# Kernel optimization log

Measured on AMD Instinct MI355X. Metric: run time of the kernel, lower is better.

Reference implementation:

```python
import jax, jax.numpy as jnp
import numpy as np

N, E = 20000, 320000
IN, OUT, H1, H2 = 256, 32, 8, 1
NEG_SLOPE = 0.2


def _gatv2(x, src, dst, Wsrc, bsrc, Wdst, bdst, attn, Wres, bres, heads, dout):
    n = x.shape[0]
    fs = (x @ Wsrc + bsrc).reshape(n, heads, dout)   # (N,H,D)
    fd = (x @ Wdst + bdst).reshape(n, heads, dout)   # (N,H,D)
    # GATv2: leaky_relu BEFORE the attention dot product
    e = jax.nn.leaky_relu(fs[src] + fd[dst], NEG_SLOPE)      # (E,H,D)
    logits = jnp.einsum('ehd,hd->eh', e, attn)               # (E,H)
    # edge softmax over destination-node segments
    m = jax.ops.segment_max(logits, dst, num_segments=n)     # (N,H)
    ex = jnp.exp(logits - m[dst])
    s = jax.ops.segment_sum(ex, dst, num_segments=n)         # (N,H)
    alpha = ex / s[dst]                                      # (E,H)
    msg = alpha[:, :, None] * fs[src]                        # (E,H,D)
    out = jax.ops.segment_sum(msg, dst, num_segments=n)      # (N,H,D)
    res = (x @ Wres + bres).reshape(n, heads, dout)          # residual (dims differ -> Linear)
    return out + res


def setup_inputs() -> dict:
    key = jax.random.key(0)
    ks = jax.random.split(key, 16)
    sc = lambda fin: 1.0 / np.sqrt(fin)
    d = {}
    d['x'] = jax.random.normal(ks[0], (N, IN), jnp.float32)
    d['src'] = jax.random.randint(ks[1], (E,), 0, N, jnp.int32)
    d['dst'] = jax.random.randint(ks[2], (E,), 0, N, jnp.int32)
    # layer 1: IN -> OUT*H1
    d['Wsrc1'] = jax.random.normal(ks[3], (IN, OUT * H1), jnp.float32) * sc(IN)
    d['bsrc1'] = jnp.zeros((OUT * H1,), jnp.float32)
    d['Wdst1'] = jax.random.normal(ks[4], (IN, OUT * H1), jnp.float32) * sc(IN)
    d['bdst1'] = jnp.zeros((OUT * H1,), jnp.float32)
    d['attn1'] = jax.random.normal(ks[5], (H1, OUT), jnp.float32) * sc(OUT)
    d['Wres1'] = jax.random.normal(ks[6], (IN, OUT * H1), jnp.float32) * sc(IN)
    d['bres1'] = jnp.zeros((OUT * H1,), jnp.float32)
    # layer 2: OUT*H1 -> OUT, 1 head
    D2 = OUT * H1
    d['Wsrc2'] = jax.random.normal(ks[7], (D2, OUT * H2), jnp.float32) * sc(D2)
    d['bsrc2'] = jnp.zeros((OUT * H2,), jnp.float32)
    d['Wdst2'] = jax.random.normal(ks[8], (D2, OUT * H2), jnp.float32) * sc(D2)
    d['bdst2'] = jnp.zeros((OUT * H2,), jnp.float32)
    d['attn2'] = jax.random.normal(ks[9], (H2, OUT), jnp.float32) * sc(OUT)
    d['Wres2'] = jax.random.normal(ks[10], (D2, OUT * H2), jnp.float32) * sc(D2)
    d['bres2'] = jnp.zeros((OUT * H2,), jnp.float32)
    return d


def reference(x, src, dst,
              Wsrc1, bsrc1, Wdst1, bdst1, attn1, Wres1, bres1,
              Wsrc2, bsrc2, Wdst2, bdst2, attn2, Wres2, bres2):
    y = _gatv2(x, src, dst, Wsrc1, bsrc1, Wdst1, bdst1, attn1, Wres1, bres1, H1, OUT)
    y = jax.nn.relu(y)                       # (N, 8, OUT)
    y = y.reshape(x.shape[0], -1)            # (N, 8*OUT)
    y = _gatv2(y, src, dst, Wsrc2, bsrc2, Wdst2, bdst2, attn2, Wres2, bres2, H2, OUT)
    return y                                  # (N, 1, OUT)
```

## Files before the change

kernel.cpp:

```cpp
#include <hip/hip_runtime.h>
#include <hip/hip_bf16.h>

#define N_NODES 20000
#define N_PAD   20096
#define N_EDGES 320000
#define D_IN    256
#define NEG     0.2f
#define MAXDEG  64
#define NSB     64
#define EPSB    5000
#define NBIN    313

typedef __attribute__((ext_vector_type(8))) short short8;
typedef __attribute__((ext_vector_type(4))) float f32x4;
typedef __attribute__((ext_vector_type(4))) unsigned short u16x4;

__device__ __forceinline__ unsigned short f2b(float f) {
    unsigned int u = __float_as_uint(f);
    unsigned int r = (u + 0x7FFFu + ((u >> 16) & 1u)) >> 16;
    return (unsigned short)r;
}
__device__ __forceinline__ float b2f(unsigned short u) {
    union { unsigned int i; float f; } v;
    v.i = ((unsigned int)u) << 16;
    return v.f;
}

__device__ __forceinline__ void gload16(const void* g, void* l) {
    __builtin_amdgcn_global_load_lds((const __attribute__((address_space(1))) void*)g,
                                     (__attribute__((address_space(3))) void*)l, 16, 0, 0);
}

#define PB1 2512
#define PB2 3280
#define PB3 3376
#define PB4 3440
#define PREP_BLOCKS 3488
__global__ __launch_bounds__(256) void k_prep(
    const float* __restrict__ x, unsigned short* __restrict__ xb,
    const float* __restrict__ Ws1, const float* __restrict__ Wd1, const float* __restrict__ Wr1,
    unsigned short* __restrict__ wt,
    const float* __restrict__ Ws2, const float* __restrict__ Wd2, const float* __restrict__ Wr2,
    unsigned short* __restrict__ wt2,
    const int* __restrict__ dst, int* __restrict__ blockhist,
    unsigned short* __restrict__ yb)
{
    int bid = blockIdx.x, tid = threadIdx.x;
    if (bid < PB1) {
        int i = bid * 256 + tid;
        int row = i >> 5, c8 = (i & 31) * 8;
        short8 v = {0, 0, 0, 0, 0, 0, 0, 0};
        if (row < N_NODES) {
            float4 a = *reinterpret_cast<const float4*>(x + (size_t)row * 256 + c8);
            float4 b = *reinterpret_cast<const float4*>(x + (size_t)row * 256 + c8 + 4);
            v[0] = (short)f2b(a.x); v[1] = (short)f2b(a.y); v[2] = (short)f2b(a.z); v[3] = (short)f2b(a.w);
            v[4] = (short)f2b(b.x); v[5] = (short)f2b(b.y); v[6] = (short)f2b(b.z); v[7] = (short)f2b(b.w);
        }
        *reinterpret_cast<short8*>(xb + (size_t)row * 256 + c8) = v;
    } else if (bid < PB2) {
        int n = bid - PB1, k = tid;
        const float* W = (n < 256) ? Ws1 : ((n < 512) ? Wd1 : Wr1);
        int c = n & 255;
        wt[(size_t)n * 256 + k] = f2b(W[(size_t)k * 256 + c]);
    } else if (bid < PB3) {
        int n = bid - PB2, k = tid;
        const float* W = (n < 32) ? Ws2 : ((n < 64) ? Wd2 : Wr2);
        int c = n & 31;
        wt2[(size_t)n * 256 + (k ^ ((n & 7) << 3))] = f2b(W[(size_t)k * 32 + c]);
    } else if (bid < PB4) {
        __shared__ int hist[NBIN];
        int blk = bid - PB3;
        for (int b = tid; b < NBIN; b += 256) hist[b] = 0;
        __syncthreads();
        for (int it = 0; it < 20; ++it) {
            int li = it * 256 + tid;
            if (li < EPSB) atomicAdd(&hist[dst[blk * EPSB + li] >> 6], 1);
        }
        __syncthreads();
        for (int b = tid; b < NBIN; b += 256) blockhist[blk * NBIN + b] = hist[b];
    } else {
        int j = (bid - PB4) * 256 + tid;
        ((unsigned int*)(yb + (size_t)N_NODES * 256))[j] = 0u;
    }
}

__global__ __launch_bounds__(320) void k_pass3(
    const int* __restrict__ src, const int* __restrict__ dst,
    const int* __restrict__ blockhist,
    unsigned long long* __restrict__ sorted,
    int* __restrict__ binbase_g, int* __restrict__ bintotal_g)
{
    __shared__ int tmp[320];
    __shared__ int binbase[NBIN];
    __shared__ int rank[NBIN];
    int blk = blockIdx.x, tid = threadIdx.x;
    int mystart = 0, total = 0;
    if (tid < NBIN) {
        for (int b = 0; b < NSB; ++b) {
            int v = blockhist[b * NBIN + tid];
            total += v;
            if (b < blk) mystart += v;
        }
    }
    tmp[tid] = (tid < NBIN) ? total : 0;
    __syncthreads();
    for (int off = 1; off < 320; off <<= 1) {
        int v = (tid >= off) ? tmp[tid - off] : 0;
        __syncthreads();
        tmp[tid] += v;
        __syncthreads();
    }
    if (tid < NBIN) {
        int excl = tmp[tid] - total;
        binbase[tid] = excl;
        rank[tid] = mystart;
        if (blk == 0) { binbase_g[tid] = excl; bintotal_g[tid] = total; }
    }
    __syncthreads();
    for (int it = 0; it < 16; ++it) {
        int li = it * 320 + tid;
        if (li < EPSB) {
            int e = blk * EPSB + li;
            int d = dst[e];
            int b = d >> 6;
            int r = atomicAdd(&rank[b], 1);
            sorted[binbase[b] + r] = ((unsigned long long)(unsigned)d << 32) | (unsigned)src[e];
        }
    }
}

#define GEMM1_BLOCKS 1884
#define PASS4_BLOCKS 313
__global__ __launch_bounds__(256) void k_gemm_l1_mfma(
    const unsigned short* __restrict__ xb,
    const unsigned short* __restrict__ wt,
    const float* __restrict__ bs, const float* __restrict__ bd, const float* __restrict__ br,
    unsigned short* __restrict__ fs, unsigned short* __restrict__ fd, unsigned short* __restrict__ res,
    const unsigned long long* __restrict__ sorted,
    const int* __restrict__ binbase_g, const int* __restrict__ bintotal_g,
    int* __restrict__ colp, int* __restrict__ cnt)
{
    __shared__ __align__(16) unsigned short SH[12288];
    int t = threadIdx.x;
    int bid = blockIdx.x;

    if (bid >= GEMM1_BLOCKS) {
        int* ch = (int*)SH;
        int nb2 = bid - GEMM1_BLOCKS;
        if (t < 64) ch[t] = 0;
        __syncthreads();
        int base = binbase_g[nb2], tot = bintotal_g[nb2];
        for (int i = t; i < tot; i += 256) {
            unsigned long long p = sorted[base + i];
            int d = (int)(p >> 32);
            int s = (int)(p & 0xffffffffULL);
            int r = atomicAdd(&ch[d & 63], 1);
            if (r < MAXDEG) colp[(size_t)d * MAXDEG + r] = s;
        }
        __syncthreads();
        int node = nb2 * 64 + t;
        if (t < 64 && node < N_NODES) cnt[node] = ch[t];
        return;
    }

    int lane = t & 63, w = t >> 6;
    const int q = 235, r = 4;
    int xcd = bid & 7, slot = bid >> 3;
    int wg = (xcd < r ? xcd * (q + 1) : r * (q + 1) + (xcd - r) * q) + slot;
    int mb = wg / 6, nb = wg % 6;
    int row0 = mb * 64;
    int which = nb >> 1;
    int col0 = (nb & 1) * 128;
    int ncol0 = nb * 128;
    unsigned short* out = (which == 0) ? fs : ((which == 1) ? fd : res);
    const float* bias   = (which == 0) ? bs : ((which == 1) ? bd : br);

    auto stage = [&](int buf, int k0) {
        char* base = (char*)SH + buf * 12288;
        {
            int c = t, row = c >> 2, kc = (c & 3) * 8;
            gload16(xb + (size_t)(row0 + row) * 256 + k0 + kc, base + c * 16);
        }
#pragma unroll
        for (int r2 = 0; r2 < 2; r2++) {
            int c = r2 * 256 + t, row = c >> 2, kc = (c & 3) * 8;
            gload16(wt + (size_t)(ncol0 + row) * 256 + k0 + kc, base + 4096 + c * 16);
        }
    };

    f32x4 acc[4][2] = {};

    stage(0, 0);
    __syncthreads();
    int cur = 0;
#pragma unroll
    for (int it = 0; it < 8; ++it) {
        if (it < 7) stage(cur ^ 1, (it + 1) * 32);
        const char* Ab = (const char*)SH + cur * 12288;
        const char* Bb = Ab + 4096;
        short8 a[4], b[2];
#pragma unroll
        for (int m = 0; m < 4; m++)
            a[m] = *reinterpret_cast<const short8*>(Ab + ((m * 16 + (lane & 15)) * 64 + (lane >> 4) * 16));
#pragma unroll
        for (int n = 0; n < 2; n++)
            b[n] = *reinterpret_cast<const short8*>(Bb + ((w * 32 + n * 16 + (lane & 15)) * 64 + (lane >> 4) * 16));
#pragma unroll
        for (int m = 0; m < 4; m++)
#pragma unroll
            for (int n = 0; n < 2; n++)
                acc[m][n] = __builtin_amdgcn_mfma_f32_16x16x32_bf16(a[m], b[n], acc[m][n], 0, 0, 0);
        __syncthreads();
        cur ^= 1;
    }

    int cgrp = lane >> 4, ccol = lane & 15;
    float bvals[2];
#pragma unroll
    for (int n = 0; n < 2; n++) bvals[n] = bias[col0 + w * 32 + n * 16 + ccol];

#pragma unroll
    for (int m = 0; m < 4; m++)
#pragma unroll
        for (int n = 0; n < 2; n++)
#pragma unroll
            for (int q2 = 0; q2 < 4; q2++) {
                int lr = m * 16 + cgrp * 4 + q2;
                int cb = (w * 32 + n * 16 + ccol) * 2;
                int addr = lr * 256 + (cb ^ (cgrp << 5));
                *(unsigned short*)((char*)SH + addr) = f2b(acc[m][n][q2] + bvals[n]);
            }
    __syncthreads();
#pragma unroll
    for (int it = 0; it < 4; it++) {
        int lr = it * 16 + (t >> 4);
        int cb = (t & 15) * 16;
        short8 v = *(const short8*)((const char*)SH + (lr * 256 + (cb ^ (((lr >> 2) & 3) << 5))));
        int gr = row0 + lr;
        if (gr < N_NODES)
            *reinterpret_cast<short8*>(out + (size_t)gr * 256 + col0 + (t & 15) * 8) = v;
    }
}

__global__ __launch_bounds__(64) void k_gather_l1(
    const int* __restrict__ cnt, const int* __restrict__ colp,
    const unsigned short* __restrict__ fs1, const unsigned short* __restrict__ fd1,
    const unsigned short* __restrict__ res1, const float* __restrict__ attn1,
    unsigned short* __restrict__ y)
{
    int n = blockIdx.x;
    int l = threadIdx.x;
    u16x4 fdv4 = *reinterpret_cast<const u16x4*>(fd1 + (size_t)n * 256 + l * 4);
    float fdv[4] = {b2f(fdv4[0]), b2f(fdv4[1]), b2f(fdv4[2]), b2f(fdv4[3])};
    float4 attv = *reinterpret_cast<const float4*>(attn1 + l * 4);
    float att[4] = {attv.x, attv.y, attv.z, attv.w};

    const int* colrow = colp + (size_t)n * MAXDEG;
    int deg = cnt[n];
    if (deg > MAXDEG) deg = MAXDEG;

    float mA = -1e30f, sA = 0.f, aA[4] = {0.f, 0.f, 0.f, 0.f};
    float mB = -1e30f, sB = 0.f, aB[4] = {0.f, 0.f, 0.f, 0.f};

    int cA0 = (0 < deg) ? colrow[0] : 0;
    int cB0 = (1 < deg) ? colrow[1] : 0;
    int cA1 = (2 < deg) ? colrow[2] : 0;
    int cB1 = (3 < deg) ? colrow[3] : 0;
    u16x4 fA  = *reinterpret_cast<const u16x4*>(fs1 + (size_t)cA0 * 256 + l * 4);
    u16x4 fB  = *reinterpret_cast<const u16x4*>(fs1 + (size_t)cB0 * 256 + l * 4);
    u16x4 fA2 = *reinterpret_cast<const u16x4*>(fs1 + (size_t)cA1 * 256 + l * 4);
    u16x4 fB2 = *reinterpret_cast<const u16x4*>(fs1 + (size_t)cB1 * 256 + l * 4);

    int idx = 0;
    for (; idx + 1 < deg; idx += 2) {
        u16x4 vA = fA, vB = fB;
        fA = fA2; fB = fB2;
        int nA = (idx + 4 < deg) ? colrow[idx + 4] : 0;
        int nB = (idx + 5 < deg) ? colrow[idx + 5] : 0;
        fA2 = *reinterpret_cast<const u16x4*>(fs1 + (size_t)nA * 256 + l * 4);
        fB2 = *reinterpret_cast<const u16x4*>(fs1 + (size_t)nB * 256 + l * 4);

        float xa0 = b2f(vA[0]), xa1 = b2f(vA[1]), xa2 = b2f(vA[2]), xa3 = b2f(vA[3]);
        float ta0 = xa0 + fdv[0]; ta0 = ta0 > 0.f ? ta0 : NEG * ta0;
        float ta1 = xa1 + fdv[1]; ta1 = ta1 > 0.f ? ta1 : NEG * ta1;
        float ta2 = xa2 + fdv[2]; ta2 = ta2 > 0.f ? ta2 : NEG * ta2;
        float ta3 = xa3 + fdv[3]; ta3 = ta3 > 0.f ? ta3 : NEG * ta3;
        float pA = ta0 * att[0] + ta1 * att[1] + ta2 * att[2] + ta3 * att[3];
        float xb0 = b2f(vB[0]), xb1 = b2f(vB[1]), xb2 = b2f(vB[2]), xb3 = b2f(vB[3]);
        float tb0 = xb0 + fdv[0]; tb0 = tb0 > 0.f ? tb0 : NEG * tb0;
        float tb1 = xb1 + fdv[1]; tb1 = tb1 > 0.f ? tb1 : NEG * tb1;
        float tb2 = xb2 + fdv[2]; tb2 = tb2 > 0.f ? tb2 : NEG * tb2;
        float tb3 = xb3 + fdv[3]; tb3 = tb3 > 0.f ? tb3 : NEG * tb3;
        float pB = tb0 * att[0] + tb1 * att[1] + tb2 * att[2] + tb3 * att[3];

        pA += __shfl_xor(pA, 1); pB += __shfl_xor(pB, 1);
        pA += __shfl_xor(pA, 2); pB += __shfl_xor(pB, 2);
        pA += __shfl_xor(pA, 4); pB += __shfl_xor(pB, 4);

        float mnA = fmaxf(mA, pA);
        float eA  = __expf(pA - mnA);
        float scA = __expf(mA - mnA);
        sA = sA * scA + eA;
        aA[0] = aA[0] * scA + eA * xa0;
        aA[1] = aA[1] * scA + eA * xa1;
        aA[2] = aA[2] * scA + eA * xa2;
        aA[3] = aA[3] * scA + eA * xa3;
        mA = mnA;

        float mnB = fmaxf(mB, pB);
        float eB  = __expf(pB - mnB);
        float scB = __expf(mB - mnB);
        sB = sB * scB + eB;
        aB[0] = aB[0] * scB + eB * xb0;
        aB[1] = aB[1] * scB + eB * xb1;
        aB[2] = aB[2] * scB + eB * xb2;
        aB[3] = aB[3] * scB + eB * xb3;
        mB = mnB;
    }
    if (idx < deg) {
        float xa0 = b2f(fA[0]), xa1 = b2f(fA[1]), xa2 = b2f(fA[2]), xa3 = b2f(fA[3]);
        float ta0 = xa0 + fdv[0]; ta0 = ta0 > 0.f ? ta0 : NEG * ta0;
        float ta1 = xa1 + fdv[1]; ta1 = ta1 > 0.f ? ta1 : NEG * ta1;
        float ta2 = xa2 + fdv[2]; ta2 = ta2 > 0.f ? ta2 : NEG * ta2;
        float ta3 = xa3 + fdv[3]; ta3 = ta3 > 0.f ? ta3 : NEG * ta3;
        float pA = ta0 * att[0] + ta1 * att[1] + ta2 * att[2] + ta3 * att[3];
        pA += __shfl_xor(pA, 1);
        pA += __shfl_xor(pA, 2);
        pA += __shfl_xor(pA, 4);
        float mnA = fmaxf(mA, pA);
        float eA  = __expf(pA - mnA);
        float scA = __expf(mA - mnA);
        sA = sA * scA + eA;
        aA[0] = aA[0] * scA + eA * xa0;
        aA[1] = aA[1] * scA + eA * xa1;
        aA[2] = aA[2] * scA + eA * xa2;
        aA[3] = aA[3] * scA + eA * xa3;
        mA = mnA;
    }
    float mn = fmaxf(mA, mB);
    float scA = __expf(mA - mn), scB = __expf(mB - mn);
    float s = sA * scA + sB * scB;
    float a0 = aA[0] * scA + aB[0] * scB;
    float a1 = aA[1] * scA + aB[1] * scB;
    float a2 = aA[2] * scA + aB[2] * scB;
    float a3 = aA[3] * scA + aB[3] * scB;

    u16x4 rv4 = *reinterpret_cast<const u16x4*>(res1 + (size_t)n * 256 + l * 4);
    float inv = (s > 0.f) ? 1.f / s : 0.f;
    u16x4 o;
    o[0] = f2b(fmaxf(a0 * inv + b2f(rv4[0]), 0.f));
    o[1] = f2b(fmaxf(a1 * inv + b2f(rv4[1]), 0.f));
    o[2] = f2b(fmaxf(a2 * inv + b2f(rv4[2]), 0.f));
    o[3] = f2b(fmaxf(a3 * inv + b2f(rv4[3]), 0.f));
    *reinterpret_cast<u16x4*>(y + (size_t)n * 256 + l * 4) = o;
}

__global__ __launch_bounds__(256) void k_gemm_l2_mfma(
    const unsigned short* __restrict__ yb,
    const unsigned short* __restrict__ wt2,
    const float* __restrict__ bs, const float* __restrict__ bd, const float* __restrict__ br,
    unsigned short* __restrict__ fs2, unsigned short* __restrict__ fd2, unsigned short* __restrict__ res2)
{
    __shared__ __align__(16) unsigned short Bs[96 * 256];
    __shared__ __align__(16) unsigned short As[2][64 * 32];
    int t = threadIdx.x;
    int lane = t & 63, w = t >> 6;
    int row0 = blockIdx.x * 64;

    auto stage_a = [&](int buf, int k0) {
        int c = t;
        int row = c >> 2, kc = (c & 3) * 8;
        gload16(yb + (size_t)(row0 + row) * 256 + k0 + kc, (char*)As[buf] + c * 16);
    };

#pragma unroll
    for (int i = 0; i < 12; i++) {
        int c = i * 256 + t;
        gload16(wt2 + (size_t)c * 8, (char*)Bs + (size_t)c * 16);
    }
    stage_a(0, 0);
    __syncthreads();

    f32x4 acc[6] = {};
    int arow0 = w * 16;
    int cur = 0;

#pragma unroll
    for (int it = 0; it < 8; ++it) {
        if (it < 7) stage_a(cur ^ 1, (it + 1) * 32);
        short8 a = *reinterpret_cast<const short8*>((const char*)As[cur] + ((arow0 + (lane & 15)) * 64 + (lane >> 4) * 16));
        short8 b[6];
#pragma unroll
        for (int n = 0; n < 6; n++) {
            int brow = n * 16 + (lane & 15);
            int kbyte = (it * 32 + (lane >> 4) * 8) * 2;
            b[n] = *reinterpret_cast<const short8*>((const char*)Bs + (brow * 512 + (kbyte ^ ((brow & 7) << 4))));
        }
#pragma unroll
        for (int n = 0; n < 6; n++)
            acc[n] = __builtin_amdgcn_mfma_f32_16x16x32_bf16(a, b[n], acc[n], 0, 0, 0);
        __syncthreads();
        cur ^= 1;
    }

    int cgrp = lane >> 4, ccol = lane & 15;
#pragma unroll
    for (int n = 0; n < 6; n++) {
        int which = n >> 1;
        int cc = (n & 1) * 16 + ccol;
        unsigned short* out = (which == 0) ? fs2 : ((which == 1) ? fd2 : res2);
        const float* bias   = (which == 0) ? bs  : ((which == 1) ? bd  : br);
        float bv = bias[cc];
        int rbase = row0 + arow0 + cgrp * 4;
#pragma unroll
        for (int q2 = 0; q2 < 4; q2++) {
            int rr = rbase + q2;
            if (rr < N_NODES) out[(size_t)rr * 32 + cc] = f2b(acc[n][q2] + bv);
        }
    }
}

__global__ __launch_bounds__(64) void k_gather_l2(
    const int* __restrict__ cnt, const int* __restrict__ colp,
    const unsigned short* __restrict__ fs2, const unsigned short* __restrict__ fd2,
    const unsigned short* __restrict__ res2, const float* __restrict__ attn2,
    float* __restrict__ out)
{
    int n = blockIdx.x;
    int l = threadIdx.x;
    int d = l & 31, h = l >> 5;
    float fdv = b2f(fd2[(size_t)n * 32 + d]);
    float att = attn2[d];
    const int* colrow = colp + (size_t)n * MAXDEG;
    int deg = cnt[n];
    if (deg > MAXDEG) deg = MAXDEG;

    float m = -1e30f, s = 0.f, acc = 0.f;
    int c0 = (h < deg) ? colrow[h] : 0;
    float fv_next = b2f(fs2[(size_t)c0 * 32 + d]);
    for (int i = h; i < deg; i += 2) {
        float fv = fv_next;
        int cn = (i + 2 < deg) ? colrow[i + 2] : 0;
        fv_next = b2f(fs2[(size_t)cn * 32 + d]);
        float t0 = fv + fdv; t0 = t0 > 0.f ? t0 : NEG * t0;
        float p = t0 * att;
        p += __shfl_xor(p, 1);
        p += __shfl_xor(p, 2);
        p += __shfl_xor(p, 4);
        p += __shfl_xor(p, 8);
        p += __shfl_xor(p, 16);
        float mn = fmaxf(m, p);
        float e  = __expf(p - mn);
        float sc = __expf(m - mn);
        s = s * sc + e;
        acc = acc * sc + e * fv;
        m = mn;
    }
    float mo = __shfl_xor(m, 32);
    float mstar = fmaxf(m, mo);
    float myc = __expf(m - mstar);
    float sp = s * myc, ap = acc * myc;
    float st = sp + __shfl_xor(sp, 32);
    float at = ap + __shfl_xor(ap, 32);
    if (l < 32) {
        float rv = b2f(res2[(size_t)n * 32 + d]);
        float inv = (st > 0.f) ? 1.f / st : 0.f;
        out[(size_t)n * 32 + d] = at * inv + rv;
    }
}

extern "C" void kernel_launch(void* const* d_in, const int* in_sizes, int n_in,
                              void* d_out, int out_size, void* d_ws, size_t ws_size,
                              hipStream_t stream)
{
    const float* x   = (const float*)d_in[0];
    const int*   src = (const int*)d_in[1];
    const int*   dst = (const int*)d_in[2];
    const float* Ws1 = (const float*)d_in[3];
    const float* bs1 = (const float*)d_in[4];
    const float* Wd1 = (const float*)d_in[5];
    const float* bd1 = (const float*)d_in[6];
    const float* at1 = (const float*)d_in[7];
    const float* Wr1 = (const float*)d_in[8];
    const float* br1 = (const float*)d_in[9];
    const float* Ws2 = (const float*)d_in[10];
    const float* bs2 = (const float*)d_in[11];
    const float* Wd2 = (const float*)d_in[12];
    const float* bd2 = (const float*)d_in[13];
    const float* at2 = (const float*)d_in[14];
    const float* Wr2 = (const float*)d_in[15];
    const float* br2 = (const float*)d_in[16];
    float* out = (float*)d_out;

    char* w = (char*)d_ws;
    size_t off = 0;
    auto alloc = [&](size_t bytes) { void* p = w + off; off += (bytes + 255) & ~(size_t)255; return p; };
    int*   cnt       = (int*)  alloc((size_t)N_NODES * 4);
    int*   colp      = (int*)  alloc((size_t)N_NODES * MAXDEG * 4);
    int*   blockhist = (int*)  alloc((size_t)NSB * NBIN * 4);
    int*   bintotal  = (int*)  alloc((size_t)NBIN * 4);
    int*   binbase   = (int*)  alloc((size_t)NBIN * 4);
    unsigned long long* sorted = (unsigned long long*)alloc((size_t)N_EDGES * 8);
    unsigned short* fs1 = (unsigned short*)alloc((size_t)N_NODES * 256 * 2);
    unsigned short* fd1 = (unsigned short*)alloc((size_t)N_NODES * 256 * 2);
    unsigned short* res1= (unsigned short*)alloc((size_t)N_NODES * 256 * 2);
    unsigned short* fs2 = (unsigned short*)alloc((size_t)N_NODES * 32 * 2);
    unsigned short* fd2 = (unsigned short*)alloc((size_t)N_NODES * 32 * 2);
    unsigned short* res2= (unsigned short*)alloc((size_t)N_NODES * 32 * 2);
    unsigned short* xb  = (unsigned short*)alloc((size_t)N_PAD * 256 * 2);
    unsigned short* yb  = (unsigned short*)alloc((size_t)N_PAD * 256 * 2);
    unsigned short* wt  = (unsigned short*)alloc((size_t)768 * 256 * 2);
    unsigned short* wt2 = (unsigned short*)alloc((size_t)96 * 256 * 2);
    (void)ws_size; (void)in_sizes; (void)n_in; (void)out_size;

    k_prep<<<PREP_BLOCKS, 256, 0, stream>>>(x, xb, Ws1, Wd1, Wr1, wt, Ws2, Wd2, Wr2, wt2,
                                            dst, blockhist, yb);
    k_pass3<<<NSB, 320, 0, stream>>>(src, dst, blockhist, sorted, binbase, bintotal);
    k_gemm_l1_mfma<<<GEMM1_BLOCKS + PASS4_BLOCKS, 256, 0, stream>>>(
        xb, wt, bs1, bd1, br1, fs1, fd1, res1, sorted, binbase, bintotal, colp, cnt);
    k_gather_l1<<<N_NODES, 64, 0, stream>>>(cnt, colp, fs1, fd1, res1, at1, yb);
    k_gemm_l2_mfma<<<N_PAD / 64, 256, 0, stream>>>(yb, wt2, bs2, bd2, br2, fs2, fd2, res2);
    k_gather_l2<<<N_NODES, 64, 0, stream>>>(cnt, colp, fs2, fd2, res2, at2, out);
}
```

Baseline: 107.1 us.

## Tile weight transpose via LDS, stage neighbor lists in LDS, use exp2

```diff
diff --git a/kernel.cpp b/kernel.cpp
--- a/kernel.cpp
+++ b/kernel.cpp
@@ -10,6 +10,7 @@
 #define NSB     64
 #define EPSB    5000
 #define NBIN    313
+#define LOG2E   1.4426950408889634f
 
 typedef __attribute__((ext_vector_type(8))) short short8;
 typedef __attribute__((ext_vector_type(4))) float f32x4;
@@ -32,10 +33,10 @@
 }
 
 #define PB1 2512
-#define PB2 3280
-#define PB3 3376
-#define PB4 3440
-#define PREP_BLOCKS 3488
+#define PB1B 2560
+#define PB2 2656
+#define PB3 2720
+#define PREP_BLOCKS 2768
 __global__ __launch_bounds__(256) void k_prep(
     const float* __restrict__ x, unsigned short* __restrict__ xb,
     const float* __restrict__ Ws1, const float* __restrict__ Wd1, const float* __restrict__ Wr1,
@@ -45,6 +46,8 @@
     const int* __restrict__ dst, int* __restrict__ blockhist,
     unsigned short* __restrict__ yb)
 {
+    __shared__ float tl[64][65];
+    __shared__ int hist[NBIN];
     int bid = blockIdx.x, tid = threadIdx.x;
     if (bid < PB1) {
         int i = bid * 256 + tid;
@@ -57,19 +60,31 @@
             v[4] = (short)f2b(b.x); v[5] = (short)f2b(b.y); v[6] = (short)f2b(b.z); v[7] = (short)f2b(b.w);
         }
         *reinterpret_cast<short8*>(xb + (size_t)row * 256 + c8) = v;
+    } else if (bid < PB1B) {
+        int b = bid - PB1;
+        int mat = b >> 4, tile = b & 15;
+        int r0 = (tile >> 2) * 64;
+        int c0 = (tile & 3) * 64;
+        const float* W = (mat == 0) ? Ws1 : ((mat == 1) ? Wd1 : Wr1);
+        int lane = tid & 63, grp = tid >> 6;
+#pragma unroll
+        for (int pass = 0; pass < 16; ++pass) {
+            int kl = pass * 4 + grp;
+            tl[kl][lane] = W[(size_t)(r0 + kl) * 256 + c0 + lane];
+        }
+        __syncthreads();
+#pragma unroll
+        for (int pass = 0; pass < 16; ++pass) {
+            int nl = pass * 4 + grp;
+            wt[(size_t)(mat * 256 + c0 + nl) * 256 + r0 + lane] = f2b(tl[lane][nl]);
+        }
     } else if (bid < PB2) {
-        int n = bid - PB1, k = tid;
-        const float* W = (n < 256) ? Ws1 : ((n < 512) ? Wd1 : Wr1);
-        int c = n & 255;
-        wt[(size_t)n * 256 + k] = f2b(W[(size_t)k * 256 + c]);
-    } else if (bid < PB3) {
-        int n = bid - PB2, k = tid;
+        int n = bid - PB1B, k = tid;
         const float* W = (n < 32) ? Ws2 : ((n < 64) ? Wd2 : Wr2);
         int c = n & 31;
         wt2[(size_t)n * 256 + (k ^ ((n & 7) << 3))] = f2b(W[(size_t)k * 32 + c]);
-    } else if (bid < PB4) {
-        __shared__ int hist[NBIN];
-        int blk = bid - PB3;
+    } else if (bid < PB3) {
+        int blk = bid - PB2;
         for (int b = tid; b < NBIN; b += 256) hist[b] = 0;
         __syncthreads();
         for (int it = 0; it < 20; ++it) {
@@ -79,7 +94,7 @@
         __syncthreads();
         for (int b = tid; b < NBIN; b += 256) blockhist[blk * NBIN + b] = hist[b];
     } else {
-        int j = (bid - PB4) * 256 + tid;
+        int j = (bid - PB3) * 256 + tid;
         ((unsigned int*)(yb + (size_t)N_NODES * 256))[j] = 0u;
     }
 }
@@ -248,49 +263,47 @@
     const unsigned short* __restrict__ res1, const float* __restrict__ attn1,
     unsigned short* __restrict__ y)
 {
+    __shared__ int slds[MAXDEG + 8];
     int n = blockIdx.x;
     int l = threadIdx.x;
+    int deg = cnt[n];
+    if (deg > MAXDEG) deg = MAXDEG;
+    slds[l] = (l < deg) ? colp[(size_t)n * MAXDEG + l] : 0;
+    if (l < 8) slds[MAXDEG + l] = 0;
+    __syncthreads();
+
     u16x4 fdv4 = *reinterpret_cast<const u16x4*>(fd1 + (size_t)n * 256 + l * 4);
     float fdv[4] = {b2f(fdv4[0]), b2f(fdv4[1]), b2f(fdv4[2]), b2f(fdv4[3])};
     float4 attv = *reinterpret_cast<const float4*>(attn1 + l * 4);
-    float att[4] = {attv.x, attv.y, attv.z, attv.w};
-
-    const int* colrow = colp + (size_t)n * MAXDEG;
-    int deg = cnt[n];
-    if (deg > MAXDEG) deg = MAXDEG;
-
-    float mA = -1e30f, sA = 0.f, aA[4] = {0.f, 0.f, 0.f, 0.f};
-    float mB = -1e30f, sB = 0.f, aB[4] = {0.f, 0.f, 0.f, 0.f};
-
-    int cA0 = (0 < deg) ? colrow[0] : 0;
-    int cB0 = (1 < deg) ? colrow[1] : 0;
-    int cA1 = (2 < deg) ? colrow[2] : 0;
-    int cB1 = (3 < deg) ? colrow[3] : 0;
-    u16x4 fA  = *reinterpret_cast<const u16x4*>(fs1 + (size_t)cA0 * 256 + l * 4);
-    u16x4 fB  = *reinterpret_cast<const u16x4*>(fs1 + (size_t)cB0 * 256 + l * 4);
-    u16x4 fA2 = *reinterpret_cast<const u16x4*>(fs1 + (size_t)cA1 * 256 + l * 4);
-    u16x4 fB2 = *reinterpret_cast<const u16x4*>(fs1 + (size_t)cB1 * 256 + l * 4);
+    float att[4] = {attv.x * LOG2E, attv.y * LOG2E, attv.z * LOG2E, attv.w * LOG2E};
+
+    float mA = -1e30f, sA = 0.f, aA0 = 0.f, aA1 = 0.f, aA2 = 0.f, aA3 = 0.f;
+    float mB = -1e30f, sB = 0.f, aB0 = 0.f, aB1 = 0.f, aB2 = 0.f, aB3 = 0.f;
+
+    u16x4 fA  = *reinterpret_cast<const u16x4*>(fs1 + (size_t)slds[0] * 256 + l * 4);
+    u16x4 fB  = *reinterpret_cast<const u16x4*>(fs1 + (size_t)slds[1] * 256 + l * 4);
+    u16x4 fA2 = *reinterpret_cast<const u16x4*>(fs1 + (size_t)slds[2] * 256 + l * 4);
+    u16x4 fB2 = *reinterpret_cast<const u16x4*>(fs1 + (size_t)slds[3] * 256 + l * 4);
 
     int idx = 0;
     for (; idx + 1 < deg; idx += 2) {
         u16x4 vA = fA, vB = fB;
         fA = fA2; fB = fB2;
-        int nA = (idx + 4 < deg) ? colrow[idx + 4] : 0;
-        int nB = (idx + 5 < deg) ? colrow[idx + 5] : 0;
-        fA2 = *reinterpret_cast<const u16x4*>(fs1 + (size_t)nA * 256 + l * 4);
-        fB2 = *reinterpret_cast<const u16x4*>(fs1 + (size_t)nB * 256 + l * 4);
+        fA2 = *reinterpret_cast<const u16x4*>(fs1 + (size_t)slds[idx + 4] * 256 + l * 4);
+        fB2 = *reinterpret_cast<const u16x4*>(fs1 + (size_t)slds[idx + 5] * 256 + l * 4);
 
         float xa0 = b2f(vA[0]), xa1 = b2f(vA[1]), xa2 = b2f(vA[2]), xa3 = b2f(vA[3]);
-        float ta0 = xa0 + fdv[0]; ta0 = ta0 > 0.f ? ta0 : NEG * ta0;
-        float ta1 = xa1 + fdv[1]; ta1 = ta1 > 0.f ? ta1 : NEG * ta1;
-        float ta2 = xa2 + fdv[2]; ta2 = ta2 > 0.f ? ta2 : NEG * ta2;
-        float ta3 = xa3 + fdv[3]; ta3 = ta3 > 0.f ? ta3 : NEG * ta3;
+        float ta0 = xa0 + fdv[0]; ta0 = fmaxf(ta0, NEG * ta0);
+        float ta1 = xa1 + fdv[1]; ta1 = fmaxf(ta1, NEG * ta1);
+        float ta2 = xa2 + fdv[2]; ta2 = fmaxf(ta2, NEG * ta2);
+        float ta3 = xa3 + fdv[3]; ta3 = fmaxf(ta3, NEG * ta3);
         float pA = ta0 * att[0] + ta1 * att[1] + ta2 * att[2] + ta3 * att[3];
+
         float xb0 = b2f(vB[0]), xb1 = b2f(vB[1]), xb2 = b2f(vB[2]), xb3 = b2f(vB[3]);
-        float tb0 = xb0 + fdv[0]; tb0 = tb0 > 0.f ? tb0 : NEG * tb0;
-        float tb1 = xb1 + fdv[1]; tb1 = tb1 > 0.f ? tb1 : NEG * tb1;
-        float tb2 = xb2 + fdv[2]; tb2 = tb2 > 0.f ? tb2 : NEG * tb2;
-        float tb3 = xb3 + fdv[3]; tb3 = tb3 > 0.f ? tb3 : NEG * tb3;
+        float tb0 = xb0 + fdv[0]; tb0 = fmaxf(tb0, NEG * tb0);
+        float tb1 = xb1 + fdv[1]; tb1 = fmaxf(tb1, NEG * tb1);
+        float tb2 = xb2 + fdv[2]; tb2 = fmaxf(tb2, NEG * tb2);
+        float tb3 = xb3 + fdv[3]; tb3 = fmaxf(tb3, NEG * tb3);
         float pB = tb0 * att[0] + tb1 * att[1] + tb2 * att[2] + tb3 * att[3];
 
         pA += __shfl_xor(pA, 1); pB += __shfl_xor(pB, 1);
@@ -298,52 +311,52 @@
         pA += __shfl_xor(pA, 4); pB += __shfl_xor(pB, 4);
 
         float mnA = fmaxf(mA, pA);
-        float eA  = __expf(pA - mnA);
-        float scA = __expf(mA - mnA);
+        float eA  = exp2f(pA - mnA);
+        float scA = exp2f(mA - mnA);
         sA = sA * scA + eA;
-        aA[0] = aA[0] * scA + eA * xa0;
-        aA[1] = aA[1] * scA + eA * xa1;
-        aA[2] = aA[2] * scA + eA * xa2;
-        aA[3] = aA[3] * scA + eA * xa3;
+        aA0 = aA0 * scA + eA * xa0;
+        aA1 = aA1 * scA + eA * xa1;
+        aA2 = aA2 * scA + eA * xa2;
+        aA3 = aA3 * scA + eA * xa3;
         mA = mnA;
 
         float mnB = fmaxf(mB, pB);
-        float eB  = __expf(pB - mnB);
-        float scB = __expf(mB - mnB);
+        float eB  = exp2f(pB - mnB);
+        float scB = exp2f(mB - mnB);
         sB = sB * scB + eB;
-        aB[0] = aB[0] * scB + eB * xb0;
-        aB[1] = aB[1] * scB + eB * xb1;
-        aB[2] = aB[2] * scB + eB * xb2;
-        aB[3] = aB[3] * scB + eB * xb3;
+        aB0 = aB0 * scB + eB * xb0;
+        aB1 = aB1 * scB + eB * xb1;
+        aB2 = aB2 * scB + eB * xb2;
+        aB3 = aB3 * scB + eB * xb3;
         mB = mnB;
     }
     if (idx < deg) {
         float xa0 = b2f(fA[0]), xa1 = b2f(fA[1]), xa2 = b2f(fA[2]), xa3 = b2f(fA[3]);
-        float ta0 = xa0 + fdv[0]; ta0 = ta0 > 0.f ? ta0 : NEG * ta0;
-        float ta1 = xa1 + fdv[1]; ta1 = ta1 > 0.f ? ta1 : NEG * ta1;
-        float ta2 = xa2 + fdv[2]; ta2 = ta2 > 0.f ? ta2 : NEG * ta2;
-        float ta3 = xa3 + fdv[3]; ta3 = ta3 > 0.f ? ta3 : NEG * ta3;
+        float ta0 = xa0 + fdv[0]; ta0 = fmaxf(ta0, NEG * ta0);
+        float ta1 = xa1 + fdv[1]; ta1 = fmaxf(ta1, NEG * ta1);
+        float ta2 = xa2 + fdv[2]; ta2 = fmaxf(ta2, NEG * ta2);
+        float ta3 = xa3 + fdv[3]; ta3 = fmaxf(ta3, NEG * ta3);
         float pA = ta0 * att[0] + ta1 * att[1] + ta2 * att[2] + ta3 * att[3];
         pA += __shfl_xor(pA, 1);
         pA += __shfl_xor(pA, 2);
         pA += __shfl_xor(pA, 4);
         float mnA = fmaxf(mA, pA);
-        float eA  = __expf(pA - mnA);
-        float scA = __expf(mA - mnA);
+        float eA  = exp2f(pA - mnA);
+        float scA = exp2f(mA - mnA);
         sA = sA * scA + eA;
-        aA[0] = aA[0] * scA + eA * xa0;
-        aA[1] = aA[1] * scA + eA * xa1;
-        aA[2] = aA[2] * scA + eA * xa2;
-        aA[3] = aA[3] * scA + eA * xa3;
+        aA0 = aA0 * scA + eA * xa0;
+        aA1 = aA1 * scA + eA * xa1;
+        aA2 = aA2 * scA + eA * xa2;
+        aA3 = aA3 * scA + eA * xa3;
         mA = mnA;
     }
     float mn = fmaxf(mA, mB);
-    float scA = __expf(mA - mn), scB = __expf(mB - mn);
-    float s = sA * scA + sB * scB;
-    float a0 = aA[0] * scA + aB[0] * scB;
-    float a1 = aA[1] * scA + aB[1] * scB;
-    float a2 = aA[2] * scA + aB[2] * scB;
-    float a3 = aA[3] * scA + aB[3] * scB;
+    float scA = exp2f(mA - mn), scB = exp2f(mB - mn);
+    float s  = sA * scA + sB * scB;
+    float a0 = aA0 * scA + aB0 * scB;
+    float a1 = aA1 * scA + aB1 * scB;
+    float a2 = aA2 * scA + aB2 * scB;
+    float a3 = aA3 * scA + aB3 * scB;
 
     u16x4 rv4 = *reinterpret_cast<const u16x4*>(res1 + (size_t)n * 256 + l * 4);
     float inv = (s > 0.f) ? 1.f / s : 0.f;
@@ -426,23 +439,24 @@
     const unsigned short* __restrict__ res2, const float* __restrict__ attn2,
     float* __restrict__ out)
 {
+    __shared__ int slds[MAXDEG + 8];
     int n = blockIdx.x;
     int l = threadIdx.x;
     int d = l & 31, h = l >> 5;
-    float fdv = b2f(fd2[(size_t)n * 32 + d]);
-    float att = attn2[d];
-    const int* colrow = colp + (size_t)n * MAXDEG;
     int deg = cnt[n];
     if (deg > MAXDEG) deg = MAXDEG;
-
+    slds[l] = (l < deg) ? colp[(size_t)n * MAXDEG + l] : 0;
+    if (l < 8) slds[MAXDEG + l] = 0;
+    __syncthreads();
+
+    float fdv = b2f(fd2[(size_t)n * 32 + d]);
+    float att = attn2[d] * LOG2E;
     float m = -1e30f, s = 0.f, acc = 0.f;
-    int c0 = (h < deg) ? colrow[h] : 0;
-    float fv_next = b2f(fs2[(size_t)c0 * 32 + d]);
+    float fv_next = b2f(fs2[(size_t)slds[h] * 32 + d]);
     for (int i = h; i < deg; i += 2) {
         float fv = fv_next;
-        int cn = (i + 2 < deg) ? colrow[i + 2] : 0;
-        fv_next = b2f(fs2[(size_t)cn * 32 + d]);
-        float t0 = fv + fdv; t0 = t0 > 0.f ? t0 : NEG * t0;
+        fv_next = b2f(fs2[(size_t)slds[i + 2] * 32 + d]);
+        float t0 = fv + fdv; t0 = fmaxf(t0, NEG * t0);
         float p = t0 * att;
         p += __shfl_xor(p, 1);
         p += __shfl_xor(p, 2);
@@ -450,15 +464,15 @@
         p += __shfl_xor(p, 8);
         p += __shfl_xor(p, 16);
         float mn = fmaxf(m, p);
-        float e  = __expf(p - mn);
-        float sc = __expf(m - mn);
+        float e  = exp2f(p - mn);
+        float sc = exp2f(m - mn);
         s = s * sc + e;
         acc = acc * sc + e * fv;
         m = mn;
     }
     float mo = __shfl_xor(m, 32);
     float mstar = fmaxf(m, mo);
-    float myc = __expf(m - mstar);
+    float myc = exp2f(m - mstar);
     float sp = s * myc, ap = acc * myc;
     float st = sp + __shfl_xor(sp, 32);
     float at = ap + __shfl_xor(ap, 32);
```

After: 108.6 us. About the same (+1.4%).
